# Kernel optimization log

Measured on AMD Instinct MI355X. Metric: run time of the kernel, lower is better.

The kernel has to match this reference:

```python
import jax, jax.numpy as jnp
import numpy as np

NQ, NKV, D = 32, 8, 64
HID = 2048
EPS = 1e-5
THETA = 1000000.0


def _rmsnorm(x, w):
    var = jnp.mean(x * x, axis=-1, keepdims=True)
    return x * jax.lax.rsqrt(var + EPS) * w


def setup_inputs() -> dict:
    key = jax.random.key(0)
    k1, k2, k3 = jax.random.split(key, 3)
    T = 2048
    positions = jnp.arange(T, dtype=jnp.int64) if jax.config.jax_enable_x64 else jnp.arange(T, dtype=jnp.int32)
    hidden_states = jax.random.normal(k1, (T, HID), dtype=jnp.float32)
    w_qkv = jax.random.normal(k2, (HID, (NQ + 2 * NKV) * D), dtype=jnp.float32) / np.sqrt(HID)
    w_out = jax.random.normal(k3, (NQ * D, HID), dtype=jnp.float32) / np.sqrt(NQ * D)
    q_ln_w = jnp.ones((D,), dtype=jnp.float32)
    k_ln_w = jnp.ones((D,), dtype=jnp.float32)
    return {"positions": positions, "hidden_states": hidden_states, "w_qkv": w_qkv,
            "w_out": w_out, "q_ln_w": q_ln_w, "k_ln_w": k_ln_w}


def reference(positions, hidden_states, w_qkv, w_out, q_ln_w, k_ln_w):
    T = hidden_states.shape[0]
    qkv = hidden_states @ w_qkv  # [T, (NQ+2*NKV)*D]
    q = qkv[:, : NQ * D].reshape(T, NQ, D)
    k = qkv[:, NQ * D : (NQ + NKV) * D].reshape(T, NKV, D)
    v = qkv[:, (NQ + NKV) * D :].reshape(T, NKV, D)
    # per-head RMSNorm on q and k
    q = _rmsnorm(q, q_ln_w)
    k = _rmsnorm(k, k_ln_w)
    # neox-style RoPE (rotate halves)
    inv_freq = 1.0 / (THETA ** (jnp.arange(0, D, 2, dtype=jnp.float32) / D))
    ang = positions.astype(jnp.float32)[:, None] * inv_freq  # [T, D/2]
    cos = jnp.cos(ang)[:, None, :]
    sin = jnp.sin(ang)[:, None, :]
    def rope(x):
        x1, x2 = x[..., : D // 2], x[..., D // 2 :]
        return jnp.concatenate([x1 * cos - x2 * sin, x2 * cos + x1 * sin], axis=-1)
    q = rope(q)
    k = rope(k)
    # grouped-query causal attention (one sequence, positions define order)
    G = NQ // NKV
    qg = q.reshape(T, NKV, G, D)
    scores = jnp.einsum('tkgd,skd->kgts', qg, k) * (D ** -0.5)  # [NKV,G,T,T]
    causal = jnp.arange(T)[:, None] >= jnp.arange(T)[None, :]
    scores = jnp.where(causal[None, None], scores, -1e30)
    probs = jax.nn.softmax(scores, axis=-1)
    attn = jnp.einsum('kgts,skd->tkgd', probs, v).reshape(T, NQ * D)
    return attn @ w_out
```

## Files before the change

kernel.cpp:

```cpp
#include <hip/hip_runtime.h>

typedef __bf16 bhalf;
typedef __bf16 bhalf8 __attribute__((ext_vector_type(8)));
typedef __bf16 bhalf4 __attribute__((ext_vector_type(4)));
typedef float f32x4 __attribute__((ext_vector_type(4)));

typedef __attribute__((address_space(1))) const void* gas_p;
typedef __attribute__((address_space(3))) void* las_p;

#define T_SEQ 2048
#define HIDN  2048
#define NQH   32
#define NKVH  8
#define DH    64
#define NQKV  3072

__global__ __launch_bounds__(256) void cast_bf16_k(const float* __restrict__ in,
                                                   bhalf* __restrict__ out, int n) {
  int i = (blockIdx.x * 256 + threadIdx.x) * 4;
  if (i + 3 < n) {
    float4 v = *(const float4*)(in + i);
    bhalf4 o;
    o[0] = (bhalf)v.x; o[1] = (bhalf)v.y; o[2] = (bhalf)v.z; o[3] = (bhalf)v.w;
    *(bhalf4*)(out + i) = o;
  }
}

__global__ __launch_bounds__(256) void transpose_cast64_k(const float* __restrict__ in,
                                                          bhalf* __restrict__ out,
                                                          int R, int C) {
  __shared__ bhalf tile[64][72];
  int tid = threadIdx.x;
  int bx = blockIdx.x * 64;
  int by = blockIdx.y * 64;
  int rl = tid >> 4, c4 = (tid & 15) * 4;
#pragma unroll
  for (int p = 0; p < 4; ++p) {
    float4 v = *(const float4*)(in + (size_t)(by + rl + 16 * p) * C + bx + c4);
    bhalf4 b;
    b[0] = (bhalf)v.x; b[1] = (bhalf)v.y; b[2] = (bhalf)v.z; b[3] = (bhalf)v.w;
    *(bhalf4*)&tile[rl + 16 * p][c4] = b;
  }
  __syncthreads();
  int c = tid >> 2, r0 = (tid & 3) * 16;
  bhalf8 o0, o1;
#pragma unroll
  for (int j = 0; j < 8; ++j) { o0[j] = tile[r0 + j][c]; o1[j] = tile[r0 + 8 + j][c]; }
  *(bhalf8*)(out + (size_t)(bx + c) * R + by + r0) = o0;
  *(bhalf8*)(out + (size_t)(bx + c) * R + by + r0 + 8) = o1;
}

__device__ __forceinline__ void gemm_core_db(const bhalf* __restrict__ A,
                                             const bhalf* __restrict__ Bt,
                                             int Kstride, int Klen,
                                             int bm, int bn, int tid,
                                             bhalf* As, bhalf* Bs, f32x4 acc[2][4]) {
  int lane = tid & 63, wv = tid >> 6;
  int m16 = lane & 15, q4 = lane >> 4;
  int srow = tid >> 3;
  int scol = ((tid & 7) ^ (srow & 7)) * 8;
  const bhalf* asrc = A + (size_t)(bm + srow) * Kstride + scol;
  const bhalf* bsrc = Bt + (size_t)(bn + srow) * Kstride + scol;
  bhalf* adst = As + (wv * 8) * 64;
  bhalf* bdst = Bs + (wv * 8) * 64;
  int swz = m16 & 7;
  int nit = Klen >> 6;

  auto stage = [&](int it) {
    int buf = it & 1, k0 = it * 64;
#pragma unroll
    for (int c = 0; c < 4; ++c)
      __builtin_amdgcn_global_load_lds((gas_p)(asrc + (size_t)(c * 32) * Kstride + k0),
                                       (las_p)(adst + buf * 8192 + c * 2048), 16, 0, 0);
#pragma unroll
    for (int c = 0; c < 2; ++c)
      __builtin_amdgcn_global_load_lds((gas_p)(bsrc + (size_t)(c * 32) * Kstride + k0),
                                       (las_p)(bdst + buf * 4096 + c * 2048), 16, 0, 0);
  };

  stage(0);
  for (int it = 0; it < nit; ++it) {
    __syncthreads();
    if (it + 1 < nit) stage(it + 1);
    const bhalf* Ab = As + (it & 1) * 8192;
    const bhalf* Bb = Bs + (it & 1) * 4096;
    bhalf8 af[2][2], bf[4][2];
#pragma unroll
    for (int mi = 0; mi < 2; ++mi)
#pragma unroll
      for (int ks = 0; ks < 2; ++ks)
        af[mi][ks] = *(const bhalf8*)&Ab[(wv * 32 + mi * 16 + m16) * 64 +
                                         (((ks * 4 + q4) ^ swz) * 8)];
#pragma unroll
    for (int ni = 0; ni < 4; ++ni)
#pragma unroll
      for (int ks = 0; ks < 2; ++ks)
        bf[ni][ks] = *(const bhalf8*)&Bb[(ni * 16 + m16) * 64 +
                                         (((ks * 4 + q4) ^ swz) * 8)];
#pragma unroll
    for (int mi = 0; mi < 2; ++mi)
#pragma unroll
      for (int ni = 0; ni < 4; ++ni) {
        acc[mi][ni] = __builtin_amdgcn_mfma_f32_16x16x32_bf16(af[mi][0], bf[ni][0], acc[mi][ni], 0, 0, 0);
        acc[mi][ni] = __builtin_amdgcn_mfma_f32_16x16x32_bf16(af[mi][1], bf[ni][1], acc[mi][ni], 0, 0, 0);
      }
  }
}

__global__ __launch_bounds__(256) void gemm1_fused_k(const bhalf* __restrict__ A,
                                                     const bhalf* __restrict__ Bt,
                                                     const int* __restrict__ pos,
                                                     const float* __restrict__ qw,
                                                     const float* __restrict__ kw,
                                                     bhalf* __restrict__ qo,
                                                     bhalf* __restrict__ ko,
                                                     bhalf* __restrict__ vt) {
  __shared__ __align__(16) bhalf As[2 * 128 * 64];
  __shared__ __align__(16) bhalf Bs[2 * 64 * 64];
  int tid = threadIdx.x, lane = tid & 63, wv = tid >> 6;
  int m16 = lane & 15, q4 = lane >> 4;
  int bm = blockIdx.y * 128, bn = blockIdx.x * 64, h = blockIdx.x;
  f32x4 zero4 = {0.f, 0.f, 0.f, 0.f};
  f32x4 acc[2][4];
#pragma unroll
  for (int mi = 0; mi < 2; ++mi)
#pragma unroll
    for (int ni = 0; ni < 4; ++ni) acc[mi][ni] = zero4;

  gemm_core_db(A, Bt, HIDN, HIDN, bm, bn, tid, As, Bs, acc);

  if (h < 40) {
    float wd[4];
    const float* wptr = (h < 32) ? qw : kw;
#pragma unroll
    for (int ni = 0; ni < 4; ++ni) wd[ni] = wptr[ni * 16 + m16];
    float f0 = exp2f((float)m16 * -0.6228615177913804f);
    float f1 = f0 * 0.001f;
#pragma unroll
    for (int mi = 0; mi < 2; ++mi)
#pragma unroll
      for (int r = 0; r < 4; ++r) {
        int trow = bm + wv * 32 + mi * 16 + q4 * 4 + r;
        float x0 = acc[mi][0][r], x1 = acc[mi][1][r], x2 = acc[mi][2][r], x3 = acc[mi][3][r];
        float ss = x0 * x0 + x1 * x1 + x2 * x2 + x3 * x3;
        ss += __shfl_xor(ss, 1);
        ss += __shfl_xor(ss, 2);
        ss += __shfl_xor(ss, 4);
        ss += __shfl_xor(ss, 8);
        float sc = rsqrtf(ss * (1.0f / 64.0f) + 1e-5f);
        float y0 = x0 * sc * wd[0], y1 = x1 * sc * wd[1];
        float y2 = x2 * sc * wd[2], y3 = x3 * sc * wd[3];
        float p = (float)pos[trow];
        float a0 = p * f0, a1 = p * f1;
        float c0 = cosf(a0), s0 = sinf(a0), c1 = cosf(a1), s1 = sinf(a1);
        float o0 = y0 * c0 - y2 * s0, o2 = y2 * c0 + y0 * s0;
        float o1 = y1 * c1 - y3 * s1, o3 = y3 * c1 + y1 * s1;
        bhalf* dst = (h < 32) ? (qo + (size_t)trow * 2048 + h * 64 + m16)
                              : (ko + (size_t)trow * 512 + (h - 32) * 64 + m16);
        dst[0] = (bhalf)o0; dst[16] = (bhalf)o1; dst[32] = (bhalf)o2; dst[48] = (bhalf)o3;
      }
  } else {
#pragma unroll
    for (int mi = 0; mi < 2; ++mi)
#pragma unroll
      for (int r = 0; r < 4; ++r) {
        int trow = bm + wv * 32 + mi * 16 + q4 * 4 + r;
#pragma unroll
        for (int ni = 0; ni < 4; ++ni)
          vt[(size_t)((h - 40) * 64 + ni * 16 + m16) * 2048 + trow] = (bhalf)acc[mi][ni][r];
      }
  }
}

__global__ __launch_bounds__(256) void gemm2_k(const bhalf* __restrict__ A,
                                               const bhalf* __restrict__ Bt,
                                               float* __restrict__ Cpart) {
  __shared__ __align__(16) bhalf As[2 * 128 * 64];
  __shared__ __align__(16) bhalf Bs[2 * 64 * 64];
  int tid = threadIdx.x, lane = tid & 63, wv = tid >> 6;
  int m16 = lane & 15, q4 = lane >> 4;
  int bm = blockIdx.y * 128, bn = blockIdx.x * 64;
  int slice = blockIdx.z;
  f32x4 zero4 = {0.f, 0.f, 0.f, 0.f};
  f32x4 acc[2][4];
#pragma unroll
  for (int mi = 0; mi < 2; ++mi)
#pragma unroll
    for (int ni = 0; ni < 4; ++ni) acc[mi][ni] = zero4;

  gemm_core_db(A + slice * 1024, Bt + slice * 1024, HIDN, 1024, bm, bn, tid, As, Bs, acc);

  float* C = Cpart + (size_t)slice * (T_SEQ * HIDN);
#pragma unroll
  for (int mi = 0; mi < 2; ++mi)
#pragma unroll
    for (int r = 0; r < 4; ++r) {
      size_t base = (size_t)(bm + wv * 32 + mi * 16 + q4 * 4 + r) * 2048 + bn + m16;
      C[base] = acc[mi][0][r]; C[base + 16] = acc[mi][1][r];
      C[base + 32] = acc[mi][2][r]; C[base + 48] = acc[mi][3][r];
    }
}

__global__ __launch_bounds__(256) void add2_k(const float* __restrict__ p0,
                                              const float* __restrict__ p1,
                                              float* __restrict__ out) {
  int i = (blockIdx.x * 256 + threadIdx.x) * 4;
  float4 a = *(const float4*)(p0 + i);
  float4 b = *(const float4*)(p1 + i);
  float4 o = {a.x + b.x, a.y + b.y, a.z + b.z, a.w + b.w};
  *(float4*)(out + i) = o;
}

__global__ __launch_bounds__(256) void attn_k(const bhalf* __restrict__ q,
                                              const bhalf* __restrict__ k,
                                              const bhalf* __restrict__ vt,
                                              bhalf* __restrict__ o) {
  __shared__ __align__(16) bhalf Kb[2][4096];
  __shared__ __align__(16) bhalf Vb[2][4096];
  __shared__ __align__(16) bhalf Pb[4][16][72];
  int tid = threadIdx.x, lane = tid & 63, w = tid >> 6;
  int h = blockIdx.x, kh = h >> 2;
  int qt = 31 - blockIdx.y;
  int qb = qt * 64;
  int m16 = lane & 15, q4 = lane >> 4;
  int wrow0 = qb + w * 16;

  const float C1 = 0.18033688011112042f;
  const float C2 = 11.541560327111707f;

  const bhalf* qp = q + (size_t)(wrow0 + m16) * 2048 + h * 64;
  bhalf8 qf0 = *(const bhalf8*)(qp + q4 * 8);
  bhalf8 qf1 = *(const bhalf8*)(qp + 32 + q4 * 8);

  int srow = tid >> 3;
  int scol = ((tid & 7) ^ (srow & 7)) * 8;
  const bhalf* ksrc = k + (size_t)srow * 512 + kh * 64 + scol;
  const bhalf* vsrc = vt + (size_t)(kh * 64 + srow) * 2048 + scol;
  bhalf* kdst = &Kb[0][0] + w * 512;
  bhalf* vdst = &Vb[0][0] + w * 512;

  auto stage = [&](int c) {
    int buf = c & 1, s0 = c * 64;
#pragma unroll
    for (int j = 0; j < 2; ++j) {
      __builtin_amdgcn_global_load_lds((gas_p)(ksrc + (size_t)(s0 + j * 32) * 512),
                                       (las_p)(kdst + buf * 4096 + j * 2048), 16, 0, 0);
      __builtin_amdgcn_global_load_lds((gas_p)(vsrc + (size_t)(j * 32) * 2048 + s0),
                                       (las_p)(vdst + buf * 4096 + j * 2048), 16, 0, 0);
    }
  };

  f32x4 zero4 = {0.f, 0.f, 0.f, 0.f};
  f32x4 oac[4];
  float psum[4] = {0.f, 0.f, 0.f, 0.f};
#pragma unroll
  for (int ni = 0; ni < 4; ++ni) oac[ni] = zero4;
  int swz = m16 & 7;

  stage(0);
  for (int c = 0; c <= qt; ++c) {
    __syncthreads();
    if (c < qt) stage(c + 1);
    int buf = c & 1, s0 = c * 64;
    if (c < qt) {
      bhalf8 kf[4][2];
#pragma unroll
      for (int st = 0; st < 4; ++st)
#pragma unroll
        for (int ks = 0; ks < 2; ++ks)
          kf[st][ks] = *(const bhalf8*)&Kb[buf][(st * 16 + m16) * 64 + (((ks * 4 + q4) ^ swz) * 8)];
      f32x4 sv[4];
#pragma unroll
      for (int st = 0; st < 4; ++st) {
        f32x4 t0 = __builtin_amdgcn_mfma_f32_16x16x32_bf16(qf0, kf[st][0], zero4, 0, 0, 0);
        sv[st] = __builtin_amdgcn_mfma_f32_16x16x32_bf16(qf1, kf[st][1], t0, 0, 0, 0);
      }
#pragma unroll
      for (int st = 0; st < 4; ++st)
#pragma unroll
        for (int r = 0; r < 4; ++r) {
          float pe = exp2f(sv[st][r] * C1 - C2);
          psum[r] += pe;
          Pb[w][q4 * 4 + r][st * 16 + m16] = (bhalf)pe;
        }
      bhalf8 vf[4][2];
#pragma unroll
      for (int ni = 0; ni < 4; ++ni)
#pragma unroll
        for (int ks = 0; ks < 2; ++ks)
          vf[ni][ks] = *(const bhalf8*)&Vb[buf][(ni * 16 + m16) * 64 + (((ks * 4 + q4) ^ swz) * 8)];
      bhalf8 ap0 = *(const bhalf8*)&Pb[w][m16][q4 * 8];
      bhalf8 ap1 = *(const bhalf8*)&Pb[w][m16][32 + q4 * 8];
#pragma unroll
      for (int ni = 0; ni < 4; ++ni) {
        oac[ni] = __builtin_amdgcn_mfma_f32_16x16x32_bf16(ap0, vf[ni][0], oac[ni], 0, 0, 0);
        oac[ni] = __builtin_amdgcn_mfma_f32_16x16x32_bf16(ap1, vf[ni][1], oac[ni], 0, 0, 0);
      }
    } else {
      bhalf8 kf[4][2];
      f32x4 sv[4];
#pragma unroll
      for (int st = 0; st < 4; ++st)
        if (st <= w) {
#pragma unroll
          for (int ks = 0; ks < 2; ++ks)
            kf[st][ks] = *(const bhalf8*)&Kb[buf][(st * 16 + m16) * 64 + (((ks * 4 + q4) ^ swz) * 8)];
          f32x4 t0 = __builtin_amdgcn_mfma_f32_16x16x32_bf16(qf0, kf[st][0], zero4, 0, 0, 0);
          sv[st] = __builtin_amdgcn_mfma_f32_16x16x32_bf16(qf1, kf[st][1], t0, 0, 0, 0);
        }
      int stwr = (w >= 2) ? 3 : 1;
#pragma unroll
      for (int st = 0; st < 4; ++st) {
        if (st > stwr) continue;
#pragma unroll
        for (int r = 0; r < 4; ++r) {
          float pe = 0.f;
          if (st <= w) {
            int trow = wrow0 + q4 * 4 + r;
            int col = s0 + st * 16 + m16;
            pe = (col <= trow) ? exp2f(sv[st][r] * C1 - C2) : 0.f;
          }
          psum[r] += pe;
          Pb[w][q4 * 4 + r][st * 16 + m16] = (bhalf)pe;
        }
      }
      int ksmax = (w >= 2) ? 1 : 0;
      bhalf8 vf[4][2];
#pragma unroll
      for (int ni = 0; ni < 4; ++ni)
#pragma unroll
        for (int ks = 0; ks < 2; ++ks)
          if (ks <= ksmax)
            vf[ni][ks] = *(const bhalf8*)&Vb[buf][(ni * 16 + m16) * 64 + (((ks * 4 + q4) ^ swz) * 8)];
      bhalf8 ap0 = *(const bhalf8*)&Pb[w][m16][q4 * 8];
#pragma unroll
      for (int ni = 0; ni < 4; ++ni)
        oac[ni] = __builtin_amdgcn_mfma_f32_16x16x32_bf16(ap0, vf[ni][0], oac[ni], 0, 0, 0);
      if (ksmax) {
        bhalf8 ap1 = *(const bhalf8*)&Pb[w][m16][32 + q4 * 8];
#pragma unroll
        for (int ni = 0; ni < 4; ++ni)
          oac[ni] = __builtin_amdgcn_mfma_f32_16x16x32_bf16(ap1, vf[ni][1], oac[ni], 0, 0, 0);
      }
    }
  }
#pragma unroll
  for (int r = 0; r < 4; ++r) {
    float ps = psum[r];
    ps += __shfl_xor(ps, 1);
    ps += __shfl_xor(ps, 2);
    ps += __shfl_xor(ps, 4);
    ps += __shfl_xor(ps, 8);
    psum[r] = 1.0f / ps;
  }
#pragma unroll
  for (int ni = 0; ni < 4; ++ni)
#pragma unroll
    for (int r = 0; r < 4; ++r) {
      int trow = wrow0 + q4 * 4 + r;
      o[(size_t)trow * 2048 + h * 64 + ni * 16 + m16] = (bhalf)(oac[ni][r] * psum[r]);
    }
}

extern "C" void kernel_launch(void* const* d_in, const int* in_sizes, int n_in,
                              void* d_out, int out_size, void* d_ws, size_t ws_size,
                              hipStream_t stream) {
  const int* positions = (const int*)d_in[0];
  const float* hidden  = (const float*)d_in[1];
  const float* w_qkv   = (const float*)d_in[2];
  const float* w_out   = (const float*)d_in[3];
  const float* q_ln    = (const float*)d_in[4];
  const float* k_ln    = (const float*)d_in[5];
  float* out = (float*)d_out;

  char* wsp = (char*)d_ws;
  bhalf* woutT   = (bhalf*)(wsp);
  bhalf* attn_bf = (bhalf*)(wsp + 8388608);
  float* part0   = (float*)(wsp + 16777216);
  float* part1   = (float*)(wsp + 33554432);
  bhalf* hid_bf  = (bhalf*)(wsp + 16777216);
  bhalf* wqkvT   = (bhalf*)(wsp + 25165824);
  bhalf* q_bf    = (bhalf*)(wsp + 50331648);
  bhalf* k_bf    = (bhalf*)(wsp + 58720256);
  bhalf* vt_g    = (bhalf*)(wsp + 60817408);

  cast_bf16_k<<<T_SEQ * HIDN / 1024, 256, 0, stream>>>(hidden, hid_bf, T_SEQ * HIDN);
  transpose_cast64_k<<<dim3(NQKV / 64, HIDN / 64), 256, 0, stream>>>(w_qkv, wqkvT, HIDN, NQKV);
  transpose_cast64_k<<<dim3(HIDN / 64, HIDN / 64), 256, 0, stream>>>(w_out, woutT, HIDN, HIDN);
  gemm1_fused_k<<<dim3(NQKV / 64, T_SEQ / 128), 256, 0, stream>>>(
      hid_bf, wqkvT, positions, q_ln, k_ln, q_bf, k_bf, vt_g);
  attn_k<<<dim3(NQH, 32), 256, 0, stream>>>(q_bf, k_bf, vt_g, attn_bf);
  gemm2_k<<<dim3(HIDN / 64, T_SEQ / 128, 2), 256, 0, stream>>>(attn_bf, woutT, part0);
  add2_k<<<T_SEQ * HIDN / 1024, 256, 0, stream>>>(part0, part1, out);
}
```

Measured before the change: 233.0 us.

## Use BK=128 single-buffered GEMM1, separate V transpose kernel, drop double buffering

GEMM1 now uses a 128-wide K tile with a single LDS buffer, and GEMM2 falls back to a single-buffered 64-wide K loop with a barrier before and after compute. The V part of the QKV output is written row-major and then transposed by a new bf16 transpose kernel, replacing the scattered strided stores in the GEMM epilogue. The aim is fewer K iterations and barriers in GEMM1 and coalesced V writes. In exchange the global-load/compute overlap from double buffering is lost and an extra kernel launch plus a V round trip through memory is added.

```diff
diff --git a/kernel.cpp b/kernel.cpp
--- a/kernel.cpp
+++ b/kernel.cpp
@@ -50,11 +50,26 @@
   *(bhalf8*)(out + (size_t)(bx + c) * R + by + r0 + 8) = o1;
 }
 
-__device__ __forceinline__ void gemm_core_db(const bhalf* __restrict__ A,
-                                             const bhalf* __restrict__ Bt,
-                                             int Kstride, int Klen,
-                                             int bm, int bn, int tid,
-                                             bhalf* As, bhalf* Bs, f32x4 acc[2][4]) {
+__global__ __launch_bounds__(256) void transpose_bf16_k(const bhalf* __restrict__ in,
+                                                        bhalf* __restrict__ out, int R, int C) {
+  __shared__ bhalf tile[32][33];
+  int bx = blockIdx.x * 32;
+  int by = blockIdx.y * 32;
+  int tx = threadIdx.x & 31, ty = threadIdx.x >> 5;
+#pragma unroll
+  for (int p = 0; p < 4; ++p)
+    tile[ty + 8 * p][tx] = in[(size_t)(by + ty + 8 * p) * C + bx + tx];
+  __syncthreads();
+#pragma unroll
+  for (int p = 0; p < 4; ++p)
+    out[(size_t)(bx + ty + 8 * p) * R + by + tx] = tile[tx][ty + 8 * p];
+}
+
+__device__ __forceinline__ void gemm_core(const bhalf* __restrict__ A,
+                                          const bhalf* __restrict__ Bt,
+                                          int Kstride, int Klen,
+                                          int bm, int bn, int tid,
+                                          bhalf* As, bhalf* Bs, f32x4 acc[2][4]) {
   int lane = tid & 63, wv = tid >> 6;
   int m16 = lane & 15, q4 = lane >> 4;
   int srow = tid >> 3;
@@ -64,38 +79,29 @@
   bhalf* adst = As + (wv * 8) * 64;
   bhalf* bdst = Bs + (wv * 8) * 64;
   int swz = m16 & 7;
-  int nit = Klen >> 6;
-
-  auto stage = [&](int it) {
-    int buf = it & 1, k0 = it * 64;
+
+  for (int k0 = 0; k0 < Klen; k0 += 64) {
 #pragma unroll
     for (int c = 0; c < 4; ++c)
       __builtin_amdgcn_global_load_lds((gas_p)(asrc + (size_t)(c * 32) * Kstride + k0),
-                                       (las_p)(adst + buf * 8192 + c * 2048), 16, 0, 0);
+                                       (las_p)(adst + c * 2048), 16, 0, 0);
 #pragma unroll
     for (int c = 0; c < 2; ++c)
       __builtin_amdgcn_global_load_lds((gas_p)(bsrc + (size_t)(c * 32) * Kstride + k0),
-                                       (las_p)(bdst + buf * 4096 + c * 2048), 16, 0, 0);
-  };
-
-  stage(0);
-  for (int it = 0; it < nit; ++it) {
+                                       (las_p)(bdst + c * 2048), 16, 0, 0);
     __syncthreads();
-    if (it + 1 < nit) stage(it + 1);
-    const bhalf* Ab = As + (it & 1) * 8192;
-    const bhalf* Bb = Bs + (it & 1) * 4096;
     bhalf8 af[2][2], bf[4][2];
 #pragma unroll
     for (int mi = 0; mi < 2; ++mi)
 #pragma unroll
       for (int ks = 0; ks < 2; ++ks)
-        af[mi][ks] = *(const bhalf8*)&Ab[(wv * 32 + mi * 16 + m16) * 64 +
+        af[mi][ks] = *(const bhalf8*)&As[(wv * 32 + mi * 16 + m16) * 64 +
                                          (((ks * 4 + q4) ^ swz) * 8)];
 #pragma unroll
     for (int ni = 0; ni < 4; ++ni)
 #pragma unroll
       for (int ks = 0; ks < 2; ++ks)
-        bf[ni][ks] = *(const bhalf8*)&Bb[(ni * 16 + m16) * 64 +
+        bf[ni][ks] = *(const bhalf8*)&Bs[(ni * 16 + m16) * 64 +
                                          (((ks * 4 + q4) ^ swz) * 8)];
 #pragma unroll
     for (int mi = 0; mi < 2; ++mi)
@@ -104,6 +110,52 @@
         acc[mi][ni] = __builtin_amdgcn_mfma_f32_16x16x32_bf16(af[mi][0], bf[ni][0], acc[mi][ni], 0, 0, 0);
         acc[mi][ni] = __builtin_amdgcn_mfma_f32_16x16x32_bf16(af[mi][1], bf[ni][1], acc[mi][ni], 0, 0, 0);
       }
+    __syncthreads();
+  }
+}
+
+__device__ __forceinline__ void gemm_core_bk128(const bhalf* __restrict__ A,
+                                                const bhalf* __restrict__ Bt,
+                                                int K, int bm, int bn, int tid,
+                                                bhalf* As, bhalf* Bs, f32x4 acc[2][4]) {
+  int lane = tid & 63, wv = tid >> 6;
+  int m16 = lane & 15, q4 = lane >> 4;
+  int srow = tid >> 4;
+  int scol = ((tid & 15) ^ (srow & 7)) * 8;
+  const bhalf* asrc = A + (size_t)(bm + srow) * K + scol;
+  const bhalf* bsrc = Bt + (size_t)(bn + srow) * K + scol;
+  bhalf* adst = As + (4 * wv) * 128;
+  bhalf* bdst = Bs + (4 * wv) * 128;
+  int swz = m16 & 7;
+
+  for (int k0 = 0; k0 < K; k0 += 128) {
+#pragma unroll
+    for (int c = 0; c < 8; ++c)
+      __builtin_amdgcn_global_load_lds((gas_p)(asrc + (size_t)(c * 16) * K + k0),
+                                       (las_p)(adst + c * 16 * 128), 16, 0, 0);
+#pragma unroll
+    for (int c = 0; c < 4; ++c)
+      __builtin_amdgcn_global_load_lds((gas_p)(bsrc + (size_t)(c * 16) * K + k0),
+                                       (las_p)(bdst + c * 16 * 128), 16, 0, 0);
+    __syncthreads();
+#pragma unroll
+    for (int ks = 0; ks < 4; ++ks) {
+      bhalf8 af[2], bf[4];
+#pragma unroll
+      for (int mi = 0; mi < 2; ++mi)
+        af[mi] = *(const bhalf8*)&As[(wv * 32 + mi * 16 + m16) * 128 +
+                                     (((ks * 4 + q4) ^ swz) * 8)];
+#pragma unroll
+      for (int ni = 0; ni < 4; ++ni)
+        bf[ni] = *(const bhalf8*)&Bs[(ni * 16 + m16) * 128 +
+                                     (((ks * 4 + q4) ^ swz) * 8)];
+#pragma unroll
+      for (int mi = 0; mi < 2; ++mi)
+#pragma unroll
+        for (int ni = 0; ni < 4; ++ni)
+          acc[mi][ni] = __builtin_amdgcn_mfma_f32_16x16x32_bf16(af[mi], bf[ni], acc[mi][ni], 0, 0, 0);
+    }
+    __syncthreads();
   }
 }
 
@@ -114,9 +166,9 @@
                                                      const float* __restrict__ kw,
                                                      bhalf* __restrict__ qo,
                                                      bhalf* __restrict__ ko,
-                                                     bhalf* __restrict__ vt) {
-  __shared__ __align__(16) bhalf As[2 * 128 * 64];
-  __shared__ __align__(16) bhalf Bs[2 * 64 * 64];
+                                                     bhalf* __restrict__ vo) {
+  __shared__ __align__(16) bhalf As[128 * 128];
+  __shared__ __align__(16) bhalf Bs[64 * 128];
   int tid = threadIdx.x, lane = tid & 63, wv = tid >> 6;
   int m16 = lane & 15, q4 = lane >> 4;
   int bm = blockIdx.y * 128, bn = blockIdx.x * 64, h = blockIdx.x;
@@ -127,7 +179,7 @@
 #pragma unroll
     for (int ni = 0; ni < 4; ++ni) acc[mi][ni] = zero4;
 
-  gemm_core_db(A, Bt, HIDN, HIDN, bm, bn, tid, As, Bs, acc);
+  gemm_core_bk128(A, Bt, HIDN, bm, bn, tid, As, Bs, acc);
 
   if (h < 40) {
     float wd[4];
@@ -165,9 +217,9 @@
 #pragma unroll
       for (int r = 0; r < 4; ++r) {
         int trow = bm + wv * 32 + mi * 16 + q4 * 4 + r;
-#pragma unroll
-        for (int ni = 0; ni < 4; ++ni)
-          vt[(size_t)((h - 40) * 64 + ni * 16 + m16) * 2048 + trow] = (bhalf)acc[mi][ni][r];
+        bhalf* dst = vo + (size_t)trow * 512 + (h - 40) * 64 + m16;
+        dst[0] = (bhalf)acc[mi][0][r]; dst[16] = (bhalf)acc[mi][1][r];
+        dst[32] = (bhalf)acc[mi][2][r]; dst[48] = (bhalf)acc[mi][3][r];
       }
   }
 }
@@ -175,8 +227,8 @@
 __global__ __launch_bounds__(256) void gemm2_k(const bhalf* __restrict__ A,
                                                const bhalf* __restrict__ Bt,
                                                float* __restrict__ Cpart) {
-  __shared__ __align__(16) bhalf As[2 * 128 * 64];
-  __shared__ __align__(16) bhalf Bs[2 * 64 * 64];
+  __shared__ __align__(16) bhalf As[128 * 64];
+  __shared__ __align__(16) bhalf Bs[64 * 64];
   int tid = threadIdx.x, lane = tid & 63, wv = tid >> 6;
   int m16 = lane & 15, q4 = lane >> 4;
   int bm = blockIdx.y * 128, bn = blockIdx.x * 64;
@@ -188,7 +240,7 @@
 #pragma unroll
     for (int ni = 0; ni < 4; ++ni) acc[mi][ni] = zero4;
 
-  gemm_core_db(A + slice * 1024, Bt + slice * 1024, HIDN, 1024, bm, bn, tid, As, Bs, acc);
+  gemm_core(A + slice * 1024, Bt + slice * 1024, HIDN, 1024, bm, bn, tid, As, Bs, acc);
 
   float* C = Cpart + (size_t)slice * (T_SEQ * HIDN);
 #pragma unroll
@@ -383,12 +435,14 @@
   bhalf* q_bf    = (bhalf*)(wsp + 50331648);
   bhalf* k_bf    = (bhalf*)(wsp + 58720256);
   bhalf* vt_g    = (bhalf*)(wsp + 60817408);
+  bhalf* v_bf    = (bhalf*)(wsp + 62914560);
 
   cast_bf16_k<<<T_SEQ * HIDN / 1024, 256, 0, stream>>>(hidden, hid_bf, T_SEQ * HIDN);
   transpose_cast64_k<<<dim3(NQKV / 64, HIDN / 64), 256, 0, stream>>>(w_qkv, wqkvT, HIDN, NQKV);
   transpose_cast64_k<<<dim3(HIDN / 64, HIDN / 64), 256, 0, stream>>>(w_out, woutT, HIDN, HIDN);
   gemm1_fused_k<<<dim3(NQKV / 64, T_SEQ / 128), 256, 0, stream>>>(
-      hid_bf, wqkvT, positions, q_ln, k_ln, q_bf, k_bf, vt_g);
+      hid_bf, wqkvT, positions, q_ln, k_ln, q_bf, k_bf, v_bf);
+  transpose_bf16_k<<<dim3(512 / 32, T_SEQ / 32), 256, 0, stream>>>(v_bf, vt_g, T_SEQ, 512);
   attn_k<<<dim3(NQH, 32), 256, 0, stream>>>(q_bf, k_bf, vt_g, attn_bf);
   gemm2_k<<<dim3(HIDN / 64, T_SEQ / 128, 2), 256, 0, stream>>>(attn_bf, woutT, part0);
   add2_k<<<T_SEQ * HIDN / 1024, 256, 0, stream>>>(part0, part1, out);
```

New measurement: 232.9 us. Within noise of the previous version (-0.1%).
